# Optimization experiments

Measured on AMD Instinct MI355X. Metric: run time of the kernel, lower is better.

Reference implementation:

```python
import jax, jax.numpy as jnp
import numpy as np

B, N_ANGLES, LR, LZ = 1, 120, 128, 192
PAD = int(np.ceil(LR * (np.sqrt(2.0) - 1.0) / 2.0))  # pad_image amount = 27
LP = LR + 2 * PAD                                     # padded plane size = 182
DELTA = 1e-11


def _rotate_plane(vol, phi):
    """Bilinear CCW rotation by phi (radians) of the (dim1, dim2) plane of
    vol [B, L, L, Z] about its center, zero fill outside (grid_sample-style)."""
    L = vol.shape[1]
    c = (L - 1) / 2.0
    g = jnp.arange(L, dtype=jnp.float32) - c
    y, x = jnp.meshgrid(g, g, indexing='ij')          # [L, L]
    cp, sp = jnp.cos(phi), jnp.sin(phi)
    sy = cp * y - sp * x + c                          # source coords (inverse map)
    sx = sp * y + cp * x + c
    y0 = jnp.floor(sy)
    x0 = jnp.floor(sx)
    wy = (sy - y0)[None, :, :, None]
    wx = (sx - x0)[None, :, :, None]
    y0i = y0.astype(jnp.int32)
    x0i = x0.astype(jnp.int32)

    def tap(yi, xi):
        valid = ((yi >= 0) & (yi < L) & (xi >= 0) & (xi < L)).astype(vol.dtype)
        v = vol[:, jnp.clip(yi, 0, L - 1), jnp.clip(xi, 0, L - 1), :]  # [B,L,L,Z]
        return v * valid[None, :, :, None]

    return ((1 - wy) * (1 - wx) * tap(y0i, x0i)
            + (1 - wy) * wx * tap(y0i, x0i + 1)
            + wy * (1 - wx) * tap(y0i + 1, x0i)
            + wy * wx * tap(y0i + 1, x0i + 1))


def _back_project(image):
    # image: [B, N_angles, Lr, Lz]
    img_p = jnp.pad(image, ((0, 0), (0, 0), (PAD, PAD), (0, 0)))   # pad_image along Lr
    slices = jnp.transpose(img_p, (1, 0, 2, 3))                     # [N, B, LP, LZ]
    angles = jnp.arange(N_ANGLES, dtype=jnp.float32) * (2.0 * jnp.pi / N_ANGLES)
    phis = 1.5 * jnp.pi - angles   # rotate_detector_z(..., negative=True): +(270deg - angle)
    ones2d = jnp.ones((1, LP, LP, 1), image.dtype)

    def body(carry, inp):
        obj, norm2d = carry
        sl, phi = inp                                               # sl: [B, LP, LZ]
        vol = jnp.broadcast_to(sl[:, None, :, :], (sl.shape[0], LP, LP, sl.shape[2]))
        rot = _rotate_plane(vol, phi)                               # [B, LP, LP, LZ]
        obj = obj + rot[:, PAD:PAD + LR, PAD:PAD + LR, :]           # unpad_object
        # norm_constant_i is all-ones, constant over batch and z -> track 2D pattern
        w = _rotate_plane(ones2d, phi)[0, PAD:PAD + LR, PAD:PAD + LR, 0]
        return (obj, norm2d + w), None

    init = (jnp.zeros((image.shape[0], LR, LR, LZ), image.dtype),
            jnp.zeros((LR, LR), image.dtype))
    (obj, norm2d), _ = jax.lax.scan(body, init, (slices, phis))
    return obj / (norm2d[None, :, :, None] + DELTA)


def setup_inputs() -> dict:
    key = jax.random.key(0)
    image = jax.random.uniform(key, (B, N_ANGLES, LR, LZ), dtype=jnp.float32)
    return {"image": image}


def reference(image):
    return _back_project(image)
```

## Files before the change

### kernel.cpp

```cpp
#include <hip/hip_runtime.h>
#include <math.h>

namespace {

constexpr int NA = 120;
constexpr int LR = 128;
constexpr int LZ = 192;
constexpr int UW2 = 182;
constexpr int ZSTR = UW2 * 16;
constexpr int ASTR = 24 * ZSTR;
constexpr float CTR = 63.5f;

typedef float v2f __attribute__((ext_vector_type(2)));

__global__ __launch_bounds__(256) void cvt9(const float* __restrict__ img,
                                            unsigned char* __restrict__ pb) {
    const int idx = blockIdx.x * 256 + threadIdx.x;
    if (idx >= NA * UW2 * 24) return;
    const int up = idx % UW2;
    const int t  = idx / UW2;
    const int zb = t % 24;
    const int a  = t / 24;
    const int z0 = zb * 8;
    const int r0 = up - 27;
    const int r1 = up - 26;

    float v0[8], v1[8];
    if (r0 >= 0 && r0 < LR) {
        const float4* p = reinterpret_cast<const float4*>(img + (a * LR + r0) * LZ + z0);
        const float4 x = p[0], y = p[1];
        v0[0]=x.x; v0[1]=x.y; v0[2]=x.z; v0[3]=x.w;
        v0[4]=y.x; v0[5]=y.y; v0[6]=y.z; v0[7]=y.w;
    } else {
#pragma unroll
        for (int j = 0; j < 8; ++j) v0[j] = 0.f;
    }
    if (r1 >= 0 && r1 < LR) {
        const float4* p = reinterpret_cast<const float4*>(img + (a * LR + r1) * LZ + z0);
        const float4 x = p[0], y = p[1];
        v1[0]=x.x; v1[1]=x.y; v1[2]=x.z; v1[3]=x.w;
        v1[4]=y.x; v1[5]=y.y; v1[6]=y.z; v1[7]=y.w;
    } else {
#pragma unroll
        for (int j = 0; j < 8; ++j) v1[j] = 0.f;
    }

    uint4 o;
    unsigned* od = &o.x;
#pragma unroll
    for (int d = 0; d < 4; ++d) {
        int w = __builtin_amdgcn_cvt_pk_fp8_f32(v0[2*d]   - 0.5f, v1[2*d]   - 0.5f, 0, false);
        w = __builtin_amdgcn_cvt_pk_fp8_f32(v0[2*d+1] - 0.5f, v1[2*d+1] - 0.5f, w, true);
        od[d] = (unsigned)w;
    }
    *reinterpret_cast<uint4*>(pb + ((size_t)a * ASTR + (size_t)zb * ZSTR + (size_t)up * 16)) = o;
}

struct __align__(8) G9 {
    float w0;
    unsigned boff;
};

__global__ __launch_bounds__(384, 6) void bp_v9(const unsigned char* __restrict__ pb,
                                                float* __restrict__ out) {
    __shared__ float2 s_cs[NA];
    __shared__ G9 s_geo[NA + 4][16];

    const int tid = threadIdx.x;

    if (tid < NA) {
        const float ang = (float)tid * (float)(2.0 * M_PI / (double)NA);
        const float phi = (float)(1.5 * M_PI) - ang;
        s_cs[tid] = make_float2(cosf(phi), sinf(phi));
    }
    __syncthreads();

    const int bid = blockIdx.x;
    const int swz = (bid & 7) * 128 + (bid >> 3);
    const int y  = swz >> 3;
    const int xg = (swz & 7) << 4;

    const float Y = (float)y - CTR;
    for (int e = tid; e < 16 * (NA + 4); e += 384) {
        const int p = e & 15;
        const int t = e >> 4;
        G9 g;
        if (t < NA) {
            const float2 cs = s_cs[t];
            const float X = (float)(xg + p) - CTR;
            const float u  = fmaf(cs.y, Y, fmaf(cs.x, X, CTR));
            const float fl = floorf(u);
            g.w0   = 1.0f - (u - fl);
            g.boff = (unsigned)(t * ASTR + ((int)fl + 27) * 16);
        } else {
            g.w0 = 0.f; g.boff = 0;
        }
        s_geo[t][p] = g;
    }
    __syncthreads();

    const int px = tid & 15;
    const int zo = tid >> 4;
    const unsigned zbase = (unsigned)(zo * ZSTR);

    v2f acc[8];
#pragma unroll
    for (int j = 0; j < 8; ++j) acc[j] = (v2f){0.f, 0.f};

    float w0r[4];
    uint4 T[4];
#pragma unroll
    for (int k = 0; k < 4; ++k) {
        const G9 g = s_geo[k][px];
        w0r[k] = g.w0;
        T[k] = *reinterpret_cast<const uint4*>(pb + (g.boff + zbase));
    }

    for (int t0 = 0; t0 < NA; t0 += 4) {
#pragma unroll
        for (int k = 0; k < 4; ++k) {
            const uint4 cur = T[k];
            const float cw0 = w0r[k];
            const G9 g = s_geo[t0 + k + 4][px];
            w0r[k] = g.w0;
            T[k] = *reinterpret_cast<const uint4*>(pb + (g.boff + zbase));
            const v2f cw = {cw0, 1.0f - cw0};
            const unsigned* q = &cur.x;
#pragma unroll
            for (int d = 0; d < 4; ++d) {
                const v2f lo = __builtin_amdgcn_cvt_pk_f32_fp8((int)q[d], false);
                const v2f hi = __builtin_amdgcn_cvt_pk_f32_fp8((int)q[d], true);
                acc[2*d + 0] = acc[2*d + 0] + cw * lo;
                acc[2*d + 1] = acc[2*d + 1] + cw * hi;
            }
        }
    }

    const float inv = (float)(1.0 / (120.0 + 1e-11));
    float* op = out + (size_t)(y * LR + xg + px) * LZ + zo * 8;
    float4 r0, r1;
    r0.x = (acc[0][0] + acc[0][1] + 60.0f) * inv;
    r0.y = (acc[1][0] + acc[1][1] + 60.0f) * inv;
    r0.z = (acc[2][0] + acc[2][1] + 60.0f) * inv;
    r0.w = (acc[3][0] + acc[3][1] + 60.0f) * inv;
    r1.x = (acc[4][0] + acc[4][1] + 60.0f) * inv;
    r1.y = (acc[5][0] + acc[5][1] + 60.0f) * inv;
    r1.z = (acc[6][0] + acc[6][1] + 60.0f) * inv;
    r1.w = (acc[7][0] + acc[7][1] + 60.0f) * inv;
    *reinterpret_cast<float4*>(op)     = r0;
    *reinterpret_cast<float4*>(op + 4) = r1;
}

struct __align__(16) Geo {
    float w0, w1;
    int b0, b1;
};

__global__ __launch_bounds__(256) void cvt_fp8(const float* __restrict__ in,
                                               unsigned int* __restrict__ out8,
                                               int n16) {
    const int i = blockIdx.x * 256 + threadIdx.x;
    if (i >= n16) return;
    const float4* p = reinterpret_cast<const float4*>(in) + (size_t)i * 4;
    uint4 o;
    unsigned int* od = &o.x;
#pragma unroll
    for (int d = 0; d < 4; ++d) {
        const float4 f = p[d];
        int w = __builtin_amdgcn_cvt_pk_fp8_f32(f.x - 0.5f, f.y - 0.5f, 0, false);
        w = __builtin_amdgcn_cvt_pk_fp8_f32(f.z - 0.5f, f.w - 0.5f, w, true);
        od[d] = (unsigned int)w;
    }
    reinterpret_cast<uint4*>(out8)[i] = o;
}

__device__ inline void blend8(v2f acc[4], float w0, float w1,
                              const uint2& t0, const uint2& t1) {
    const v2f W0 = {w0, w0};
    const v2f W1 = {w1, w1};
    const unsigned int* q0 = &t0.x;
    const unsigned int* q1 = &t1.x;
#pragma unroll
    for (int d = 0; d < 2; ++d) {
        const v2f a_lo = __builtin_amdgcn_cvt_pk_f32_fp8((int)q0[d], false);
        const v2f a_hi = __builtin_amdgcn_cvt_pk_f32_fp8((int)q0[d], true);
        const v2f b_lo = __builtin_amdgcn_cvt_pk_f32_fp8((int)q1[d], false);
        const v2f b_hi = __builtin_amdgcn_cvt_pk_f32_fp8((int)q1[d], true);
        acc[2 * d + 0] = acc[2 * d + 0] + W0 * a_lo + W1 * b_lo;
        acc[2 * d + 1] = acc[2 * d + 1] + W0 * a_hi + W1 * b_hi;
    }
}

__global__ __launch_bounds__(192, 6) void bp_v5(const unsigned char* __restrict__ img,
                                                float* __restrict__ out) {
    __shared__ float2 s_cs[NA];
    __shared__ Geo s_geo[NA][8];
    __shared__ float s_sumw[8];

    const int tid = threadIdx.x;
    if (tid < NA) {
        const float ang = (float)tid * (float)(2.0 * M_PI / (double)NA);
        const float phi = (float)(1.5 * M_PI) - ang;
        s_cs[tid] = make_float2(cosf(phi), sinf(phi));
    }
    __syncthreads();

    const int bid = blockIdx.x;
    const int swz = (bid & 7) * 256 + (bid >> 3);
    const int y  = swz >> 4;
    const int xg = (swz & 15) << 3;

    const float Y = (float)y - CTR;
    for (int e = tid; e < 8 * NA; e += 192) {
        const int p = e & 7;
        const int a = e >> 3;
        const float2 cs = s_cs[a];
        const float X = (float)(xg + p) - CTR;
        const float u  = fmaf(cs.y, Y, fmaf(cs.x, X, CTR));
        const float fl = floorf(u);
        const float wx = u - fl;
        const int i0 = (int)fl;
        Geo g;
        g.w0 = ((unsigned)i0 < 128u) ? (1.0f - wx) : 0.0f;
        g.w1 = ((unsigned)(i0 + 1) < 128u) ? wx : 0.0f;
        const int o0 = min(max(i0, 0), LR - 1);
        const int o1 = min(max(i0 + 1, 0), LR - 1);
        g.b0 = (a * LR + o0) * LZ;
        g.b1 = (a * LR + o1) * LZ;
        s_geo[a][p] = g;
    }
    __syncthreads();

    if (tid < 8) {
        float s = 0.f;
        for (int a = 0; a < NA; ++a) s += s_geo[a][tid].w0 + s_geo[a][tid].w1;
        s_sumw[tid] = s;
    }
    __syncthreads();

    const int zo = tid % 24;
    const int px = tid / 24;
    const unsigned char* base = img + zo * 8;

    v2f acc[4];
#pragma unroll
    for (int j = 0; j < 4; ++j) acc[j] = (v2f){0.f, 0.f};

    Geo ga = s_geo[0][px];
    Geo gb = s_geo[1][px];
    uint2 A0 = *reinterpret_cast<const uint2*>(base + ga.b0);
    uint2 A1 = *reinterpret_cast<const uint2*>(base + ga.b1);
    uint2 B0 = *reinterpret_cast<const uint2*>(base + gb.b0);
    uint2 B1 = *reinterpret_cast<const uint2*>(base + gb.b1);

    for (int a = 0; a < NA - 2; a += 2) {
        const Geo gn = s_geo[a + 2][px];
        const uint2 N0 = *reinterpret_cast<const uint2*>(base + gn.b0);
        const uint2 N1 = *reinterpret_cast<const uint2*>(base + gn.b1);
        blend8(acc, ga.w0, ga.w1, A0, A1);
        ga = gn; A0 = N0; A1 = N1;
        const Geo gm = s_geo[a + 3][px];
        const uint2 M0 = *reinterpret_cast<const uint2*>(base + gm.b0);
        const uint2 M1 = *reinterpret_cast<const uint2*>(base + gm.b1);
        blend8(acc, gb.w0, gb.w1, B0, B1);
        gb = gm; B0 = M0; B1 = M1;
    }
    blend8(acc, ga.w0, ga.w1, A0, A1);
    blend8(acc, gb.w0, gb.w1, B0, B1);

    const float inv = (float)(1.0 / (120.0 + 1e-11));
    const float half_sw = 0.5f * s_sumw[px];
    float* op = out + ((size_t)(y * LR + xg + px)) * LZ + zo * 8;
    float4 r0, r1;
    r0.x = (acc[0][0] + half_sw) * inv;
    r0.y = (acc[0][1] + half_sw) * inv;
    r0.z = (acc[1][0] + half_sw) * inv;
    r0.w = (acc[1][1] + half_sw) * inv;
    r1.x = (acc[2][0] + half_sw) * inv;
    r1.y = (acc[2][1] + half_sw) * inv;
    r1.z = (acc[3][0] + half_sw) * inv;
    r1.w = (acc[3][1] + half_sw) * inv;
    *reinterpret_cast<float4*>(op)     = r0;
    *reinterpret_cast<float4*>(op + 4) = r1;
}

__global__ __launch_bounds__(192) void bp_main(const float* __restrict__ img,
                                               float* __restrict__ out) {
    __shared__ float s_cp[NA];
    __shared__ float s_sp[NA];
    struct __align__(16) GeoF { float w0, w1; int off0, off1; };
    __shared__ GeoF s_geo[4][NA];

    const int tx = threadIdx.x;
    const int py = threadIdx.y;
    const int tid = py * 48 + tx;
    const int y  = blockIdx.x >> 5;
    const int xg = (blockIdx.x & 31) << 2;

    if (tid < NA) {
        const float ang = (float)tid * (float)(2.0 * M_PI / (double)NA);
        const float phi = (float)(1.5 * M_PI) - ang;
        s_cp[tid] = cosf(phi);
        s_sp[tid] = sinf(phi);
    }
    __syncthreads();

    for (int e = tid; e < 4 * NA; e += 192) {
        const int a = e % NA;
        const int p = e / NA;
        const float cp = s_cp[a];
        const float sp = s_sp[a];
        const float Yf = (float)y - CTR;
        const float Xf = (float)(xg + p) - CTR;
        const float u = sp * Yf + cp * Xf + CTR;
        const float fl = floorf(u);
        const float wx = u - fl;
        const int i0 = (int)fl;
        GeoF g;
        g.w0 = (i0 >= 0 && i0 < LR) ? (1.0f - wx) : 0.0f;
        g.w1 = (i0 >= -1 && i0 < LR - 1) ? wx : 0.0f;
        const int o0 = min(max(i0, 0), LR - 1);
        const int o1 = min(max(i0 + 1, 0), LR - 1);
        g.off0 = (a * LR + o0) * LZ;
        g.off1 = (a * LR + o1) * LZ;
        s_geo[p][a] = g;
    }
    __syncthreads();

    const int zb = tx << 2;
    float4 acc = make_float4(0.f, 0.f, 0.f, 0.f);
#pragma unroll 4
    for (int a = 0; a < NA; ++a) {
        const GeoF g = s_geo[py][a];
        const float4 v0 = *reinterpret_cast<const float4*>(img + g.off0 + zb);
        const float4 v1 = *reinterpret_cast<const float4*>(img + g.off1 + zb);
        acc.x = fmaf(g.w0, v0.x, fmaf(g.w1, v1.x, acc.x));
        acc.y = fmaf(g.w0, v0.y, fmaf(g.w1, v1.y, acc.y));
        acc.z = fmaf(g.w0, v0.z, fmaf(g.w1, v1.z, acc.z));
        acc.w = fmaf(g.w0, v0.w, fmaf(g.w1, v1.w, acc.w));
    }
    const float inv = (float)(1.0 / (120.0 + 1e-11));
    float4 r;
    r.x = acc.x * inv; r.y = acc.y * inv; r.z = acc.z * inv; r.w = acc.w * inv;
    *reinterpret_cast<float4*>(out + (y * LR + xg + py) * LZ + zb) = r;
}

}

extern "C" void kernel_launch(void* const* d_in, const int* in_sizes, int n_in,
                              void* d_out, int out_size, void* d_ws, size_t ws_size,
                              hipStream_t stream) {
    const float* img = (const float*)d_in[0];
    float* out = (float*)d_out;
    const int n = NA * LR * LZ;
    const size_t v9_bytes  = (size_t)NA * ASTR;
    const size_t fp8_bytes = (size_t)n;

    if (ws_size >= v9_bytes) {
        unsigned char* pb = (unsigned char*)d_ws;
        const int nt = NA * UW2 * 24;
        hipLaunchKernelGGL(cvt9, dim3((nt + 255) / 256), dim3(256), 0, stream,
                           img, pb);
        hipLaunchKernelGGL(bp_v9, dim3(1024), dim3(384), 0, stream, pb, out);
    } else if (ws_size >= fp8_bytes) {
        unsigned int* img8 = (unsigned int*)d_ws;
        const int n16 = n / 16;
        hipLaunchKernelGGL(cvt_fp8, dim3((n16 + 255) / 256), dim3(256), 0, stream,
                           img, img8, n16);
        hipLaunchKernelGGL(bp_v5, dim3(128 * 16), dim3(192), 0, stream,
                           (const unsigned char*)img8, out);
    } else {
        hipLaunchKernelGGL(bp_main, dim3(128 * 32), dim3(48, 4), 0, stream,
                           img, out);
    }
}
```

Baseline: 50.91 us.

## Split z range across blocks and force packed FMA via inline asm

The main back-projection kernel now uses 192-thread blocks that each cover half of the z range, so four times as many blocks are launched and each block recomputes the shared geometry table for its half. The swizzle mapping from block index to (y, x-group, z-half) is changed to match. Accumulation uses inline v_pk_fma_f32 assembly so the compiler emits a fused packed multiply-add rather than separate multiply and add. The smaller blocks aim for better occupancy and load balance, at the cost of doubling the per-block geometry setup relative to useful work.

```diff
diff --git a/kernel.cpp b/kernel.cpp
--- a/kernel.cpp
+++ b/kernel.cpp
@@ -12,6 +12,10 @@
 constexpr float CTR = 63.5f;
 
 typedef float v2f __attribute__((ext_vector_type(2)));
+
+__device__ inline void pk_fma(v2f& acc, v2f w, v2f t) {
+    asm("v_pk_fma_f32 %0, %1, %2, %0" : "+v"(acc) : "v"(w), "v"(t));
+}
 
 __global__ __launch_bounds__(256) void cvt9(const float* __restrict__ img,
                                             unsigned char* __restrict__ pb) {
@@ -56,15 +60,15 @@
     *reinterpret_cast<uint4*>(pb + ((size_t)a * ASTR + (size_t)zb * ZSTR + (size_t)up * 16)) = o;
 }
 
-struct __align__(8) G9 {
+struct __align__(8) G11 {
     float w0;
     unsigned boff;
 };
 
-__global__ __launch_bounds__(384, 6) void bp_v9(const unsigned char* __restrict__ pb,
-                                                float* __restrict__ out) {
+__global__ __launch_bounds__(192, 8) void bp_v11(const unsigned char* __restrict__ pb,
+                                                 float* __restrict__ out) {
     __shared__ float2 s_cs[NA];
-    __shared__ G9 s_geo[NA + 4][16];
+    __shared__ G11 s_geo[NA + 4][16];
 
     const int tid = threadIdx.x;
 
@@ -76,15 +80,16 @@
     __syncthreads();
 
     const int bid = blockIdx.x;
-    const int swz = (bid & 7) * 128 + (bid >> 3);
-    const int y  = swz >> 3;
-    const int xg = (swz & 7) << 4;
+    const int swz = (bid & 7) * 512 + (bid >> 3);
+    const int y  = swz >> 5;
+    const int xg = ((swz >> 1) & 7) << 4;
+    const int zh = swz & 1;
 
     const float Y = (float)y - CTR;
-    for (int e = tid; e < 16 * (NA + 4); e += 384) {
+    for (int e = tid; e < 16 * (NA + 4); e += 192) {
         const int p = e & 15;
         const int t = e >> 4;
-        G9 g;
+        G11 g;
         if (t < NA) {
             const float2 cs = s_cs[t];
             const float X = (float)(xg + p) - CTR;
@@ -101,18 +106,18 @@
 
     const int px = tid & 15;
     const int zo = tid >> 4;
-    const unsigned zbase = (unsigned)(zo * ZSTR);
+    const unsigned zbase = (unsigned)((zh * 12 + zo) * ZSTR);
 
     v2f acc[8];
 #pragma unroll
     for (int j = 0; j < 8; ++j) acc[j] = (v2f){0.f, 0.f};
 
-    float w0r[4];
+    float wr[4];
     uint4 T[4];
 #pragma unroll
     for (int k = 0; k < 4; ++k) {
-        const G9 g = s_geo[k][px];
-        w0r[k] = g.w0;
+        const G11 g = s_geo[k][px];
+        wr[k] = g.w0;
         T[k] = *reinterpret_cast<const uint4*>(pb + (g.boff + zbase));
     }
 
@@ -120,9 +125,9 @@
 #pragma unroll
         for (int k = 0; k < 4; ++k) {
             const uint4 cur = T[k];
-            const float cw0 = w0r[k];
-            const G9 g = s_geo[t0 + k + 4][px];
-            w0r[k] = g.w0;
+            const float cw0 = wr[k];
+            const G11 g = s_geo[t0 + k + 4][px];
+            wr[k] = g.w0;
             T[k] = *reinterpret_cast<const uint4*>(pb + (g.boff + zbase));
             const v2f cw = {cw0, 1.0f - cw0};
             const unsigned* q = &cur.x;
@@ -130,14 +135,14 @@
             for (int d = 0; d < 4; ++d) {
                 const v2f lo = __builtin_amdgcn_cvt_pk_f32_fp8((int)q[d], false);
                 const v2f hi = __builtin_amdgcn_cvt_pk_f32_fp8((int)q[d], true);
-                acc[2*d + 0] = acc[2*d + 0] + cw * lo;
-                acc[2*d + 1] = acc[2*d + 1] + cw * hi;
+                pk_fma(acc[2*d + 0], cw, lo);
+                pk_fma(acc[2*d + 1], cw, hi);
             }
         }
     }
 
     const float inv = (float)(1.0 / (120.0 + 1e-11));
-    float* op = out + (size_t)(y * LR + xg + px) * LZ + zo * 8;
+    float* op = out + (size_t)(y * LR + xg + px) * LZ + (zh * 12 + zo) * 8;
     float4 r0, r1;
     r0.x = (acc[0][0] + acc[0][1] + 60.0f) * inv;
     r0.y = (acc[1][0] + acc[1][1] + 60.0f) * inv;
@@ -353,15 +358,15 @@
     const float* img = (const float*)d_in[0];
     float* out = (float*)d_out;
     const int n = NA * LR * LZ;
-    const size_t v9_bytes  = (size_t)NA * ASTR;
+    const size_t v11_bytes = (size_t)NA * ASTR;
     const size_t fp8_bytes = (size_t)n;
 
-    if (ws_size >= v9_bytes) {
+    if (ws_size >= v11_bytes) {
         unsigned char* pb = (unsigned char*)d_ws;
         const int nt = NA * UW2 * 24;
         hipLaunchKernelGGL(cvt9, dim3((nt + 255) / 256), dim3(256), 0, stream,
                            img, pb);
-        hipLaunchKernelGGL(bp_v9, dim3(1024), dim3(384), 0, stream, pb, out);
+        hipLaunchKernelGGL(bp_v11, dim3(4096), dim3(192), 0, stream, pb, out);
     } else if (ws_size >= fp8_bytes) {
         unsigned int* img8 = (unsigned int*)d_ws;
         const int n16 = n / 16;
```

Result: slower. 82.67 us (+62.4%).
